# Optimization experiments

Hardware: AMD Instinct MI355X
Metric: run time of the kernel (lower is better)

Reference implementation:

```python
import jax, jax.numpy as jnp
import numpy as np

SCALE = 1.0 / np.sqrt(512.0).astype(np.float32)  # attention() hardcodes d_k=512


def setup_inputs() -> dict:
    key = jax.random.key(0)
    ks = jax.random.split(key, 9)
    B, S, D = 4, 2048, 512
    mk = lambda k, shape: jax.random.normal(k, shape, dtype=jnp.float32) * 0.05
    return {
        "q": mk(ks[0], (B, S, D)),
        "k": mk(ks[1], (B, S, D)),
        "v": mk(ks[2], (B, S, D)),
        "WQ_w": mk(ks[3], (D, D)),
        "WQ_b": mk(ks[4], (D,)),
        "WK_w": mk(ks[5], (D, D)),
        "WK_b": mk(ks[6], (D,)),
        "WV_w": mk(ks[7], (D, D)),
        "WV_b": mk(ks[8], (D,)),
    }


def reference(q, k, v, WQ_w, WQ_b, WK_w, WK_b, WV_w, WV_b):
    # torch nn.Linear: y = x @ W.T + b
    qp = q @ WQ_w.T + WQ_b  # [B,S,dk]
    kp = k @ WK_w.T + WK_b  # [B,S,dk]
    vp = v @ WV_w.T + WV_b  # [B,S,dv]
    qk = jnp.einsum("bqd,bkd->bqk", qp, kp) * SCALE  # [B,Sq,Sk]
    S = qk.shape[1]
    tril = jnp.tril(jnp.ones((S, S), dtype=qk.dtype))  # multiplicative causal mask
    qk = qk * tril
    # NOTE: original applies softmax over dim=1 (the query axis), faithfully kept.
    attn = jax.nn.softmax(qk, axis=1)
    out = jnp.einsum("bqk,bkd->bqd", attn, vp)  # [B,Sq,dv]
    return out
```

## Files before the change

### kernel.cpp

```cpp
#include <hip/hip_runtime.h>
#include <hip/hip_bf16.h>


#define S_LEN 2048
#define D_DIM 512
#define SCALE_F 0.044194173824159216f

typedef __attribute__((ext_vector_type(8))) short s8v;
typedef __attribute__((ext_vector_type(4))) short s4v;
typedef __attribute__((ext_vector_type(4))) float f4v;

enum { EPI_BIAS = 0, EPI_BIAS_T = 1, EPI_SCORES = 2 };

#define SBAR()    asm volatile("s_barrier" ::: "memory")
#define WAITV(n)  asm volatile("s_waitcnt vmcnt(" #n ")" ::: "memory")

__device__ __forceinline__ short f2bf_s(float f) {
  union { __hip_bfloat16 b; short s; } u; u.b = __float2bfloat16(f); return u.s;
}
__device__ __forceinline__ float bf2f_s(short h) {
  union { short s; __hip_bfloat16 b; } u; u.s = h; return __bfloat162float(u.b);
}

__device__ __forceinline__ void glds16(const short* g, short* l) {
  __builtin_amdgcn_global_load_lds((const __attribute__((address_space(1))) void*)g,
                                   (__attribute__((address_space(3))) void*)l, 16, 0, 0);
}

template <int EPI>
__device__ __forceinline__ void gemm_core(
    const short* __restrict__ A, const short* __restrict__ B,
    short* __restrict__ C, const float* __restrict__ bias,
    short* SMEM, int N, int K, size_t sCz, int m0, int n0, int bz,
    float* __restrict__ Z)
{
  const int tid  = threadIdx.x;
  const int w    = tid >> 6;
  const int lane = tid & 63;
  const int quad = lane >> 4;
  const int l16  = lane & 15;
  const int wm   = (w >> 1) * 64;
  const int wn   = (w & 1) * 64;

  const int strow = tid >> 3;
  const int gl = ((tid & 7) ^ (strow & 7)) * 8;

  f4v acc[4][4];
#pragma unroll
  for (int i = 0; i < 4; ++i)
#pragma unroll
    for (int j = 0; j < 4; ++j)
#pragma unroll
      for (int r = 0; r < 4; ++r) acc[i][j][r] = 0.0f;

  const short* Ag = A + (size_t)(m0 + strow) * K + gl;
  const short* Bg = B + (size_t)(n0 + strow) * K + gl;
  const size_t pstr = (size_t)32 * K;
  const int t8 = tid * 8;
  const int swq = l16 & 7;

  const int niter = K >> 6;

#pragma unroll
  for (int p = 0; p < 4; ++p) glds16(Ag + p * pstr, SMEM + t8 + p * 2048);
#pragma unroll
  for (int p = 0; p < 4; ++p) glds16(Bg + p * pstr, SMEM + 8192 + t8 + p * 2048);

  for (int i = 0; i < niter; ++i) {
    const int c = i & 1;
    if (i + 1 < niter) {
      const int k1 = (i + 1) << 6;
      short* dA = SMEM + (1 - c) * 16384 + t8;
#pragma unroll
      for (int p = 0; p < 4; ++p) glds16(Ag + k1 + p * pstr, dA + p * 2048);
#pragma unroll
      for (int p = 0; p < 4; ++p) glds16(Bg + k1 + p * pstr, dA + 8192 + p * 2048);
      WAITV(8);
    } else {
      WAITV(0);
    }
    SBAR();

    const short* As = SMEM + c * 16384;
    const short* Bs = As + 8192;
#pragma unroll
    for (int kk = 0; kk < 2; ++kk) {
      s8v af[4], bf[4];
#pragma unroll
      for (int ii = 0; ii < 4; ++ii)
        af[ii] = *(const s8v*)&As[(wm + ii * 16 + l16) * 64 + (((kk * 4 + quad) ^ swq) * 8)];
#pragma unroll
      for (int j = 0; j < 4; ++j)
        bf[j] = *(const s8v*)&Bs[(wn + j * 16 + l16) * 64 + (((kk * 4 + quad) ^ swq) * 8)];
#pragma unroll
      for (int ii = 0; ii < 4; ++ii)
#pragma unroll
        for (int j = 0; j < 4; ++j)
          acc[ii][j] = __builtin_amdgcn_mfma_f32_16x16x32_bf16(af[ii], bf[j], acc[ii][j], 0, 0, 0);
    }
    SBAR();
  }

  float bv[4];
  if (EPI == EPI_BIAS || EPI == EPI_BIAS_T) {
#pragma unroll
    for (int j = 0; j < 4; ++j) bv[j] = bias[n0 + wn + j * 16 + l16];
  }

  if (EPI == EPI_BIAS_T) {
#pragma unroll
    for (int i = 0; i < 4; ++i) {
#pragma unroll
      for (int j = 0; j < 4; ++j) {
        const int gn  = n0 + wn + j * 16 + l16;
        const int gmb = m0 + wm + i * 16 + quad * 4;
        const int bb = gmb >> 11, ssb = gmb & (S_LEN - 1);
        s4v o;
#pragma unroll
        for (int r = 0; r < 4; ++r) o[r] = f2bf_s(acc[i][j][r] + bv[j]);
        *(s4v*)&C[((size_t)bb * D_DIM + gn) * S_LEN + ssb] = o;
      }
    }
    return;
  }

  short* TB = SMEM;
  const int wbase = w * 2176;
  float csum[4] = {0.f, 0.f, 0.f, 0.f};

#pragma unroll
  for (int ph = 0; ph < 2; ++ph) {
    __syncthreads();
#pragma unroll
    for (int ii = 0; ii < 2; ++ii) {
      const int i = ph * 2 + ii;
#pragma unroll
      for (int j = 0; j < 4; ++j) {
        const int gn = n0 + wn + j * 16 + l16;
#pragma unroll
        for (int r = 0; r < 4; ++r) {
          short o;
          if (EPI == EPI_SCORES) {
            const int gm = m0 + wm + i * 16 + quad * 4 + r;
            const float e = (gm >= gn) ? __expf(acc[i][j][r] * SCALE_F) : 1.0f;
            csum[j] += e;
            o = f2bf_s(e);
          } else {
            o = f2bf_s(acc[i][j][r] + bv[j]);
          }
          TB[wbase + (ii * 16 + quad * 4 + r) * 68 + j * 16 + l16] = o;
        }
      }
    }
    __syncthreads();
#pragma unroll
    for (int p = 0; p < 4; ++p) {
      const int row = p * 8 + (lane >> 3);
      const int cg  = lane & 7;
      const s8v vv = *(const s8v*)&TB[wbase + row * 68 + cg * 8];
      const int gm = m0 + wm + ph * 32 + row;
      const int gn = n0 + wn + cg * 8;
      *(s8v*)&C[sCz + (size_t)gm * N + gn] = vv;
    }
  }

  if (EPI == EPI_SCORES) {
#pragma unroll
    for (int j = 0; j < 4; ++j) {
      float cs = csum[j];
      cs += __shfl_xor(cs, 16, 64);
      cs += __shfl_xor(cs, 32, 64);
      if (quad == 0) atomicAdd(&Z[(bz << 11) + n0 + wn + j * 16 + l16], cs);
    }
  }
}

__global__ __launch_bounds__(256, 2) void gemm_scores(
    const short* __restrict__ A, const short* __restrict__ B, short* __restrict__ C,
    float* __restrict__ Z)
{
  __shared__ __align__(16) short SMEM[32768];
  const int bz = blockIdx.z;
  gemm_core<EPI_SCORES>(A + (size_t)bz * S_LEN * D_DIM, B + (size_t)bz * S_LEN * D_DIM,
                        C, nullptr, SMEM, S_LEN, D_DIM,
                        (size_t)bz * S_LEN * S_LEN, blockIdx.y * 128, blockIdx.x * 128,
                        bz, Z);
}

__global__ __launch_bounds__(256, 2) void proj3(
    const short* __restrict__ a0, const short* __restrict__ a1, const short* __restrict__ a2,
    const short* __restrict__ b0, const short* __restrict__ b1, const short* __restrict__ b2,
    short* __restrict__ c0, short* __restrict__ c1, short* __restrict__ c2,
    const float* __restrict__ x0, const float* __restrict__ x1, const float* __restrict__ x2)
{
  __shared__ __align__(16) short SMEM[32768];
  const int z = blockIdx.z;
  const short* A = (z == 0) ? a0 : (z == 1) ? a1 : a2;
  const short* B = (z == 0) ? b0 : (z == 1) ? b1 : b2;
  short*       C = (z == 0) ? c0 : (z == 1) ? c1 : c2;
  const float* bias = (z == 0) ? x0 : (z == 1) ? x1 : x2;
  if (z == 2)
    gemm_core<EPI_BIAS_T>(A, B, C, bias, SMEM, D_DIM, D_DIM, 0,
                          blockIdx.y * 128, blockIdx.x * 128, 0, nullptr);
  else
    gemm_core<EPI_BIAS>(A, B, C, bias, SMEM, D_DIM, D_DIM, 0,
                        blockIdx.y * 128, blockIdx.x * 128, 0, nullptr);
}

__global__ __launch_bounds__(256, 2) void gemm_out(
    const short* __restrict__ E, const short* __restrict__ vpT,
    float* __restrict__ out)
{
  __shared__ __align__(16) short SMEM[36864];

  const int tid  = threadIdx.x;
  const int bz   = blockIdx.z;
  const int m0   = blockIdx.y * 64;
  const int n0   = blockIdx.x * 128;

  const short* A = E   + (size_t)bz * S_LEN * S_LEN;
  const short* B = vpT + (size_t)bz * D_DIM * S_LEN;

  const int w    = tid >> 6;
  const int lane = tid & 63;
  const int quad = lane >> 4;
  const int l16  = lane & 15;
  const int wm   = (w >> 1) * 32;
  const int wn   = (w & 1) * 64;

  const int strow = tid >> 3;
  const int gl = ((tid & 7) ^ (strow & 7)) * 8;

  f4v acc[2][4];
#pragma unroll
  for (int i = 0; i < 2; ++i)
#pragma unroll
    for (int j = 0; j < 4; ++j)
#pragma unroll
      for (int r = 0; r < 4; ++r) acc[i][j][r] = 0.0f;

  const short* Ag = A + (size_t)(m0 + strow) * S_LEN + gl;
  const short* Bg = B + (size_t)(n0 + strow) * S_LEN + gl;
  const size_t pstr = (size_t)32 * S_LEN;
  const int t8 = tid * 8;
  const int swq = l16 & 7;

  const int niter = S_LEN >> 6;

#pragma unroll
  for (int pre = 0; pre < 2; ++pre) {
    short* dst = SMEM + pre * 12288 + t8;
    const int k0 = pre << 6;
#pragma unroll
    for (int p = 0; p < 2; ++p) glds16(Ag + k0 + p * pstr, dst + p * 2048);
#pragma unroll
    for (int p = 0; p < 4; ++p) glds16(Bg + k0 + p * pstr, dst + 4096 + p * 2048);
  }

  int cbuf = 0, nbuf = 2;
  for (int i = 0; i < niter; ++i) {
    if (i + 2 < niter) {
      const int k2 = (i + 2) << 6;
      short* dst = SMEM + nbuf * 12288 + t8;
#pragma unroll
      for (int p = 0; p < 2; ++p) glds16(Ag + k2 + p * pstr, dst + p * 2048);
#pragma unroll
      for (int p = 0; p < 4; ++p) glds16(Bg + k2 + p * pstr, dst + 4096 + p * 2048);
      nbuf = (nbuf == 2) ? 0 : nbuf + 1;
      WAITV(12);
    } else if (i + 1 < niter) {
      WAITV(6);
    } else {
      WAITV(0);
    }
    SBAR();

    const short* As = SMEM + cbuf * 12288;
    const short* Bs = As + 4096;
    cbuf = (cbuf == 2) ? 0 : cbuf + 1;
#pragma unroll
    for (int kk = 0; kk < 2; ++kk) {
      s8v af[2], bf[4];
#pragma unroll
      for (int ii = 0; ii < 2; ++ii)
        af[ii] = *(const s8v*)&As[(wm + ii * 16 + l16) * 64 + (((kk * 4 + quad) ^ swq) * 8)];
#pragma unroll
      for (int j = 0; j < 4; ++j)
        bf[j] = *(const s8v*)&Bs[(wn + j * 16 + l16) * 64 + (((kk * 4 + quad) ^ swq) * 8)];
#pragma unroll
      for (int ii = 0; ii < 2; ++ii)
#pragma unroll
        for (int j = 0; j < 4; ++j)
          acc[ii][j] = __builtin_amdgcn_mfma_f32_16x16x32_bf16(af[ii], bf[j], acc[ii][j], 0, 0, 0);
    }
    SBAR();
  }

  float* Cf = out + (size_t)bz * S_LEN * D_DIM;
#pragma unroll
  for (int i = 0; i < 2; ++i) {
#pragma unroll
    for (int j = 0; j < 4; ++j) {
      const int gn = n0 + wn + j * 16 + l16;
#pragma unroll
      for (int r = 0; r < 4; ++r) {
        const int gm = m0 + wm + i * 16 + quad * 4 + r;
        Cf[(size_t)gm * D_DIM + gn] = acc[i][j][r];
      }
    }
  }
}

__global__ __launch_bounds__(256) void cvt3(
    const float* __restrict__ s0, const float* __restrict__ s1,
    const float* __restrict__ s2, short* __restrict__ dst, int n)
{
  const float* s = (blockIdx.y == 0) ? s0 : (blockIdx.y == 1) ? s1 : s2;
  short* d = dst + (size_t)blockIdx.y * n;
  const int i = (blockIdx.x * 256 + threadIdx.x) * 8;
  if (i >= n) return;
  const float4 f0 = *(const float4*)(s + i);
  const float4 f1 = *(const float4*)(s + i + 4);
  s8v o;
  o[0] = f2bf_s(f0.x); o[1] = f2bf_s(f0.y); o[2] = f2bf_s(f0.z); o[3] = f2bf_s(f0.w);
  o[4] = f2bf_s(f1.x); o[5] = f2bf_s(f1.y); o[6] = f2bf_s(f1.z); o[7] = f2bf_s(f1.w);
  *(s8v*)(d + i) = o;
}

__global__ __launch_bounds__(256) void scale_vpt(
    short* __restrict__ vpT, const float* __restrict__ Z)
{
  const size_t base = ((size_t)blockIdx.x * 256 + threadIdx.x) * 8;
  const int kk = (int)(base & (S_LEN - 1));
  const int b  = (int)(base >> 20);
  const float4 z0 = *(const float4*)&Z[(b << 11) + kk];
  const float4 z1 = *(const float4*)&Z[(b << 11) + kk + 4];
  s8v v = *(s8v*)&vpT[base];
  v[0] = f2bf_s(bf2f_s(v[0]) / z0.x); v[1] = f2bf_s(bf2f_s(v[1]) / z0.y);
  v[2] = f2bf_s(bf2f_s(v[2]) / z0.z); v[3] = f2bf_s(bf2f_s(v[3]) / z0.w);
  v[4] = f2bf_s(bf2f_s(v[4]) / z1.x); v[5] = f2bf_s(bf2f_s(v[5]) / z1.y);
  v[6] = f2bf_s(bf2f_s(v[6]) / z1.z); v[7] = f2bf_s(bf2f_s(v[7]) / z1.w);
  *(s8v*)&vpT[base] = v;
}

extern "C" void kernel_launch(void* const* d_in, const int* in_sizes, int n_in,
                              void* d_out, int out_size, void* d_ws, size_t ws_size,
                              hipStream_t stream) {
  const float* q   = (const float*)d_in[0];
  const float* k   = (const float*)d_in[1];
  const float* v   = (const float*)d_in[2];
  const float* WQw = (const float*)d_in[3];
  const float* WQb = (const float*)d_in[4];
  const float* WKw = (const float*)d_in[5];
  const float* WKb = (const float*)d_in[6];
  const float* WVw = (const float*)d_in[7];
  const float* WVb = (const float*)d_in[8];

  char* ws = (char*)d_ws;
  short* E   = (short*)(ws);
  short* qb  = (short*)(ws);
  short* Wqb = (short*)(ws + 25165824);
  short* qp  = (short*)(ws + 33554432);
  short* kp  = (short*)(ws + 41943040);
  short* vpT = (short*)(ws + 50331648);
  float* Z   = (float*)(ws + 58720256);
  short* kb  = qb + 4194304;
  short* vb  = qb + 8388608;
  short* Wkb = Wqb + 262144;
  short* Wvb = Wqb + 524288;

  const dim3 blk(256);

  hipMemsetAsync(Z, 0, 4 * S_LEN * sizeof(float), stream);

  cvt3<<<dim3(2048, 3), blk, 0, stream>>>(q, k, v, qb, 4194304);
  cvt3<<<dim3(128, 3), blk, 0, stream>>>(WQw, WKw, WVw, Wqb, 262144);

  proj3<<<dim3(4, 64, 3), blk, 0, stream>>>(
      qb, kb, vb, Wqb, Wkb, Wvb, qp, kp, vpT, WQb, WKb, WVb);

  gemm_scores<<<dim3(16, 16, 4), blk, 0, stream>>>(qp, kp, E, Z);

  scale_vpt<<<dim3(2048), blk, 0, stream>>>(vpT, Z);

  gemm_out<<<dim3(4, 32, 4), blk, 0, stream>>>(E, vpT, (float*)d_out);
}
```

Measured before the change: 198.3 us.

## Exploit causal mask structure by factoring exp into (exp-1)+1 and skipping upper-triangle tiles

Masked score entries equal exp(0)=1, so each column's softmax is rewritten as (e-1) on the lower triangle plus a constant term of 1 everywhere. The scores GEMM now launches only the 136 lower-triangular 128x128 tiles per batch, and the output GEMM iterates K only up to the diagonal. The constant part is folded in as a per-column sum Tv of the scaled V, which a new reduction kernel computes while it also scales vpT by 1/(2048+Z). Roughly half the score and output GEMM work is removed. The cost is an sqrt-based triangular index decode, an extra reduction, and bf16 storage of exp-1 values.

```diff
diff --git a/kernel.cpp b/kernel.cpp
--- a/kernel.cpp
+++ b/kernel.cpp
@@ -142,9 +142,9 @@
           short o;
           if (EPI == EPI_SCORES) {
             const int gm = m0 + wm + i * 16 + quad * 4 + r;
-            const float e = (gm >= gn) ? __expf(acc[i][j][r] * SCALE_F) : 1.0f;
-            csum[j] += e;
-            o = f2bf_s(e);
+            const float f = (gm >= gn) ? (__expf(acc[i][j][r] * SCALE_F) - 1.0f) : 0.0f;
+            csum[j] += f;
+            o = f2bf_s(f);
           } else {
             o = f2bf_s(acc[i][j][r] + bv[j]);
           }
@@ -175,16 +175,20 @@
   }
 }
 
-__global__ __launch_bounds__(256, 2) void gemm_scores(
+__global__ __launch_bounds__(256, 2) void gemm_scoresF(
     const short* __restrict__ A, const short* __restrict__ B, short* __restrict__ C,
     float* __restrict__ Z)
 {
   __shared__ __align__(16) short SMEM[32768];
   const int bz = blockIdx.z;
+  const int t = blockIdx.x;
+  int ti = (int)((sqrtf(8.0f * t + 1.0f) - 1.0f) * 0.5f);
+  while ((ti + 1) * (ti + 2) / 2 <= t) ++ti;
+  while (ti * (ti + 1) / 2 > t) --ti;
+  const int tj = t - ti * (ti + 1) / 2;
   gemm_core<EPI_SCORES>(A + (size_t)bz * S_LEN * D_DIM, B + (size_t)bz * S_LEN * D_DIM,
                         C, nullptr, SMEM, S_LEN, D_DIM,
-                        (size_t)bz * S_LEN * S_LEN, blockIdx.y * 128, blockIdx.x * 128,
-                        bz, Z);
+                        (size_t)bz * S_LEN * S_LEN, ti * 128, tj * 128, bz, Z);
 }
 
 __global__ __launch_bounds__(256, 2) void proj3(
@@ -207,18 +211,18 @@
                         blockIdx.y * 128, blockIdx.x * 128, 0, nullptr);
 }
 
-__global__ __launch_bounds__(256, 2) void gemm_out(
-    const short* __restrict__ E, const short* __restrict__ vpT,
-    float* __restrict__ out)
+__global__ __launch_bounds__(256, 2) void gemm_outF(
+    const short* __restrict__ F, const short* __restrict__ vpT,
+    const float* __restrict__ Tv, float* __restrict__ out)
 {
   __shared__ __align__(16) short SMEM[36864];
 
   const int tid  = threadIdx.x;
   const int bz   = blockIdx.z;
-  const int m0   = blockIdx.y * 64;
+  const int m0   = (31 - blockIdx.y) * 64;
   const int n0   = blockIdx.x * 128;
 
-  const short* A = E   + (size_t)bz * S_LEN * S_LEN;
+  const short* A = F   + (size_t)bz * S_LEN * S_LEN;
   const short* B = vpT + (size_t)bz * D_DIM * S_LEN;
 
   const int w    = tid >> 6;
@@ -245,7 +249,7 @@
   const int t8 = tid * 8;
   const int swq = l16 & 7;
 
-  const int niter = S_LEN >> 6;
+  const int niter = (m0 >> 6) + 1;
 
 #pragma unroll
   for (int pre = 0; pre < 2; ++pre) {
@@ -302,10 +306,11 @@
 #pragma unroll
     for (int j = 0; j < 4; ++j) {
       const int gn = n0 + wn + j * 16 + l16;
+      const float tvn = Tv[(bz << 9) + gn];
 #pragma unroll
       for (int r = 0; r < 4; ++r) {
         const int gm = m0 + wm + i * 16 + quad * 4 + r;
-        Cf[(size_t)gm * D_DIM + gn] = acc[i][j][r];
+        Cf[(size_t)gm * D_DIM + gn] = acc[i][j][r] + tvn;
       }
     }
   }
@@ -327,20 +332,30 @@
   *(s8v*)(d + i) = o;
 }
 
-__global__ __launch_bounds__(256) void scale_vpt(
-    short* __restrict__ vpT, const float* __restrict__ Z)
-{
-  const size_t base = ((size_t)blockIdx.x * 256 + threadIdx.x) * 8;
-  const int kk = (int)(base & (S_LEN - 1));
-  const int b  = (int)(base >> 20);
-  const float4 z0 = *(const float4*)&Z[(b << 11) + kk];
-  const float4 z1 = *(const float4*)&Z[(b << 11) + kk + 4];
-  s8v v = *(s8v*)&vpT[base];
-  v[0] = f2bf_s(bf2f_s(v[0]) / z0.x); v[1] = f2bf_s(bf2f_s(v[1]) / z0.y);
-  v[2] = f2bf_s(bf2f_s(v[2]) / z0.z); v[3] = f2bf_s(bf2f_s(v[3]) / z0.w);
-  v[4] = f2bf_s(bf2f_s(v[4]) / z1.x); v[5] = f2bf_s(bf2f_s(v[5]) / z1.y);
-  v[6] = f2bf_s(bf2f_s(v[6]) / z1.z); v[7] = f2bf_s(bf2f_s(v[7]) / z1.w);
-  *(s8v*)&vpT[base] = v;
+__global__ __launch_bounds__(256) void scale_vpt_T(
+    short* __restrict__ vpT, const float* __restrict__ ZF, float* __restrict__ Tv)
+{
+  __shared__ float red[4];
+  const int b = blockIdx.y, d = blockIdx.x, tid = threadIdx.x;
+  const size_t rowbase = ((size_t)(b * D_DIM + d)) * S_LEN;
+  const float* zf = ZF + (b << 11);
+  const int k0 = tid * 8;
+
+  s8v v = *(s8v*)&vpT[rowbase + k0];
+  float s = 0.0f;
+#pragma unroll
+  for (int i = 0; i < 8; ++i) {
+    const float w = bf2f_s(v[i]) / (2048.0f + zf[k0 + i]);
+    s += w;
+    v[i] = f2bf_s(w);
+  }
+  *(s8v*)&vpT[rowbase + k0] = v;
+
+#pragma unroll
+  for (int off = 32; off >= 1; off >>= 1) s += __shfl_xor(s, off, 64);
+  if ((tid & 63) == 0) red[tid >> 6] = s;
+  __syncthreads();
+  if (tid == 0) Tv[(b << 9) + d] = red[0] + red[1] + red[2] + red[3];
 }
 
 extern "C" void kernel_launch(void* const* d_in, const int* in_sizes, int n_in,
@@ -357,13 +372,14 @@
   const float* WVb = (const float*)d_in[8];
 
   char* ws = (char*)d_ws;
-  short* E   = (short*)(ws);
+  short* F   = (short*)(ws);
   short* qb  = (short*)(ws);
   short* Wqb = (short*)(ws + 25165824);
   short* qp  = (short*)(ws + 33554432);
   short* kp  = (short*)(ws + 41943040);
   short* vpT = (short*)(ws + 50331648);
-  float* Z   = (float*)(ws + 58720256);
+  float* ZF  = (float*)(ws + 58720256);
+  float* Tv  = (float*)(ws + 58753024);
   short* kb  = qb + 4194304;
   short* vb  = qb + 8388608;
   short* Wkb = Wqb + 262144;
@@ -371,7 +387,7 @@
 
   const dim3 blk(256);
 
-  hipMemsetAsync(Z, 0, 4 * S_LEN * sizeof(float), stream);
+  hipMemsetAsync(ZF, 0, 4 * S_LEN * sizeof(float), stream);
 
   cvt3<<<dim3(2048, 3), blk, 0, stream>>>(q, k, v, qb, 4194304);
   cvt3<<<dim3(128, 3), blk, 0, stream>>>(WQw, WKw, WVw, Wqb, 262144);
@@ -379,9 +395,9 @@
   proj3<<<dim3(4, 64, 3), blk, 0, stream>>>(
       qb, kb, vb, Wqb, Wkb, Wvb, qp, kp, vpT, WQb, WKb, WVb);
 
-  gemm_scores<<<dim3(16, 16, 4), blk, 0, stream>>>(qp, kp, E, Z);
-
-  scale_vpt<<<dim3(2048), blk, 0, stream>>>(vpT, Z);
-
-  gemm_out<<<dim3(4, 32, 4), blk, 0, stream>>>(E, vpT, (float*)d_out);
-}
+  gemm_scoresF<<<dim3(136, 1, 4), blk, 0, stream>>>(qp, kp, F, ZF);
+
+  scale_vpt_T<<<dim3(512, 4), blk, 0, stream>>>(vpT, ZF, Tv);
+
+  gemm_outF<<<dim3(4, 32, 4), blk, 0, stream>>>(F, vpT, Tv, (float*)d_out);
+}
```

Result: faster. 183.2 us (-7.6%).
